# Performance work log

Measured on AMD Instinct MI355X. Metric: run time of the kernel, lower is better.

The kernel has to match this reference:

```python
import jax, jax.numpy as jnp
import numpy as np

N = 50000
E = 600000
HIDDEN = 128
HEADS = 4
HEAD_DIM = HIDDEN // HEADS
NEG_SLOPE = 0.2
LN_EPS = 1e-5


def setup_inputs() -> dict:
    key = jax.random.key(0)
    ks = jax.random.split(key, 16)
    s = 1.0 / np.sqrt(HIDDEN)
    inp = {
        "h": jax.random.normal(ks[0], (N, HIDDEN), dtype=jnp.float32),
        "src": jax.random.randint(ks[1], (E,), 0, N, dtype=jnp.int32),
        "dst": jax.random.randint(ks[2], (E,), 0, N, dtype=jnp.int32),
        # GATv2 params (share_weights=False, bias=True)
        "W_src": jax.random.normal(ks[3], (HIDDEN, HIDDEN), dtype=jnp.float32) * s,
        "b_src": jnp.zeros((HIDDEN,), dtype=jnp.float32),
        "W_dst": jax.random.normal(ks[4], (HIDDEN, HIDDEN), dtype=jnp.float32) * s,
        "b_dst": jnp.zeros((HIDDEN,), dtype=jnp.float32),
        "attn": jax.random.normal(ks[5], (HEADS, HEAD_DIM), dtype=jnp.float32) * s,
        # FFN params
        "W1": jax.random.normal(ks[6], (HIDDEN, 2 * HIDDEN), dtype=jnp.float32) * s,
        "bf1": jnp.zeros((2 * HIDDEN,), dtype=jnp.float32),
        "W2": jax.random.normal(ks[7], (2 * HIDDEN, HIDDEN), dtype=jnp.float32) * (1.0 / np.sqrt(2 * HIDDEN)),
        "bf2": jnp.zeros((HIDDEN,), dtype=jnp.float32),
        # LayerNorms
        "g1": jnp.ones((HIDDEN,), dtype=jnp.float32),
        "beta1": jnp.zeros((HIDDEN,), dtype=jnp.float32),
        "g2": jnp.ones((HIDDEN,), dtype=jnp.float32),
        "beta2": jnp.zeros((HIDDEN,), dtype=jnp.float32),
    }
    return inp


def _layernorm(x, g, b):
    mu = jnp.mean(x, axis=-1, keepdims=True)
    var = jnp.mean(jnp.square(x - mu), axis=-1, keepdims=True)
    return (x - mu) * jax.lax.rsqrt(var + LN_EPS) * g + b


def reference(h, src, dst, W_src, b_src, W_dst, b_dst, attn,
              W1, bf1, W2, bf2, g1, beta1, g2, beta2):
    # --- GATv2 attention (eval mode, dropouts are identity) ---
    fs = (h @ W_src + b_src).reshape(N, HEADS, HEAD_DIM)   # [N,H,D]
    fd = (h @ W_dst + b_dst).reshape(N, HEADS, HEAD_DIM)
    e = jax.nn.leaky_relu(fs[src] + fd[dst], NEG_SLOPE)    # [E,H,D]
    logits = jnp.einsum('ehd,hd->eh', e, attn)             # [E,H]
    # edge softmax over incoming edges of each dst node
    m = jax.ops.segment_max(logits, dst, num_segments=N)   # [N,H]
    m = jnp.where(jnp.isfinite(m), m, 0.0)                 # guard zero-in-degree
    a = jnp.exp(logits - m[dst])                           # [E,H]
    denom = jax.ops.segment_sum(a, dst, num_segments=N)    # [N,H]
    denom = jnp.where(denom == 0.0, 1.0, denom)
    alpha = a / denom[dst]                                 # [E,H]
    msg = fs[src] * alpha[:, :, None]                      # [E,H,D]
    rst = jax.ops.segment_sum(msg, dst, num_segments=N)    # [N,H,D]
    h_attn = rst.reshape(N, HIDDEN)
    # --- residual + LN, FFN + residual + LN ---
    h1 = _layernorm(h + h_attn, g1, beta1)
    ffn = jax.nn.gelu(h1 @ W1 + bf1, approximate=False) @ W2 + bf2
    out = _layernorm(h1 + ffn, g2, beta2)
    return out
```

## Files before the change

kernel.cpp:

```cpp
#include <hip/hip_runtime.h>
#include <math.h>

#define N_NODES 50000
#define N_EDGES 600000
#define HID 128
#define FFN_HID 256
#define NEG_SLOPE 0.2f
#define LN_EPS 1e-5f
#define BKT 64

typedef unsigned short u16;
typedef unsigned int u32;
typedef __attribute__((ext_vector_type(8))) short short8;
typedef __attribute__((ext_vector_type(4))) float floatx4;

__device__ __forceinline__ u16 f2bf(float x) {
    unsigned int u = __float_as_uint(x);
    unsigned int r = u + 0x7FFFu + ((u >> 16) & 1u);
    return (u16)(r >> 16);
}
__device__ __forceinline__ float bflo(u32 u) { return __uint_as_float(u << 16); }
__device__ __forceinline__ float bfhi(u32 u) { return __uint_as_float(u & 0xffff0000u); }
__device__ __forceinline__ u32 packbf(float lo, float hi) {
    return (u32)f2bf(lo) | ((u32)f2bf(hi) << 16);
}
__device__ __forceinline__ float gelu_fast(float v) {
    float u = 1.5957691216057308f * fmaf(0.044715f * v * v, v, v);
    return v / (1.0f + __expf(-u));
}


__global__ void scatter_prep(const int* __restrict__ src, const int* __restrict__ dst,
                             int* __restrict__ cursor, u16* __restrict__ ebkt,
                             const float* __restrict__ Wsrc, const float* __restrict__ Wdst,
                             const float* __restrict__ W1, const float* __restrict__ W2,
                             u16* __restrict__ B1, u16* __restrict__ B2, u16* __restrict__ B3) {
    int b = blockIdx.x;
    if (b < 2344) {
        int e = b * 256 + threadIdx.x;
        if (e < N_EDGES) {
            int d = dst[e];
            int slot = atomicAdd(&cursor[d], 1);
            if (slot < BKT) ebkt[(size_t)d * BKT + slot] = (u16)src[e];
        }
        return;
    }
    int t = (b - 2344) * 256 + threadIdx.x;
    const float* W; u16* out; int K, Nc, noff;
    if (t < 16384)       { W = Wsrc; out = B1; K = 128; Nc = 128; noff = 0; }
    else if (t < 32768)  { W = Wdst; out = B1; K = 128; Nc = 128; noff = 128; t -= 16384; }
    else if (t < 65536)  { W = W1;   out = B2; K = 128; Nc = 256; noff = 0;   t -= 32768; }
    else if (t < 98304)  { W = W2;   out = B3; K = 256; Nc = 128; noff = 0;   t -= 65536; }
    else return;
    int n = t % Nc, k = t / Nc;
    int ng = noff + n;
    int ksteps = K >> 5;
    int frag = (ng >> 4) * ksteps + (k >> 5);
    int lane = ((k >> 3) & 3) * 16 + (ng & 15);
    int j = k & 7;
    out[((size_t)frag * 64 + lane) * 8 + j] = f2bf(W[(size_t)k * Nc + n]);
}


__global__ __launch_bounds__(256) void gemm_fsfd_mfma(
    const float* __restrict__ h, const u16* __restrict__ Bsw,
    const float* __restrict__ bsrc, const float* __restrict__ bdst,
    u16* __restrict__ fsb, float* __restrict__ fdf)
{
    int tid = threadIdx.x, wave = tid >> 6, lane = tid & 63;
    int lrow = lane & 15, lq = lane >> 4;
    short8 bfrag[4][4];
    #pragma unroll
    for (int nt = 0; nt < 4; nt++)
        #pragma unroll
        for (int ks = 0; ks < 4; ks++) {
            int frag = (wave * 4 + nt) * 4 + ks;
            bfrag[nt][ks] = *(const short8*)(Bsw + ((size_t)frag * 64 + lane) * 8);
        }
    float bias[4];
    #pragma unroll
    for (int nt = 0; nt < 4; nt++) {
        int cg = wave * 64 + nt * 16 + lrow;
        bias[nt] = (cg < HID) ? bsrc[cg] : bdst[cg - HID];
    }
    for (int mb = blockIdx.x; mb < N_NODES / 16; mb += gridDim.x) {
        int m0 = mb * 16;
        const float* hrow = h + (size_t)(m0 + lrow) * HID;
        floatx4 acc[4];
        #pragma unroll
        for (int nt = 0; nt < 4; nt++) acc[nt] = {0.f, 0.f, 0.f, 0.f};
        #pragma unroll
        for (int ks = 0; ks < 4; ks++) {
            float4 va = *(const float4*)(hrow + ks * 32 + lq * 8);
            float4 vb = *(const float4*)(hrow + ks * 32 + lq * 8 + 4);
            short8 a;
            a[0] = (short)f2bf(va.x); a[1] = (short)f2bf(va.y);
            a[2] = (short)f2bf(va.z); a[3] = (short)f2bf(va.w);
            a[4] = (short)f2bf(vb.x); a[5] = (short)f2bf(vb.y);
            a[6] = (short)f2bf(vb.z); a[7] = (short)f2bf(vb.w);
            #pragma unroll
            for (int nt = 0; nt < 4; nt++)
                acc[nt] = __builtin_amdgcn_mfma_f32_16x16x32_bf16(a, bfrag[nt][ks], acc[nt], 0, 0, 0);
        }
        #pragma unroll
        for (int nt = 0; nt < 4; nt++) {
            int cg = wave * 64 + nt * 16 + lrow;
            if (cg < HID) {
                #pragma unroll
                for (int r = 0; r < 4; r++) {
                    int row = m0 + lq * 4 + r;
                    fsb[(size_t)row * HID + cg] = f2bf(acc[nt][r] + bias[nt]);
                }
            } else {
                #pragma unroll
                for (int r = 0; r < 4; r++) {
                    int row = m0 + lq * 4 + r;
                    fdf[(size_t)row * HID + cg - HID] = acc[nt][r] + bias[nt];
                }
            }
        }
    }
}


__global__ __launch_bounds__(256) void aggregate_kernel(
    const u16* __restrict__ fsb, const float* __restrict__ fdf,
    const float* __restrict__ h, const float* __restrict__ attn,
    const int* __restrict__ counts, const u16* __restrict__ ebkt,
    const float* __restrict__ g1, const float* __restrict__ beta1,
    float* __restrict__ h1f, u16* __restrict__ h1b)
{
    int wave = threadIdx.x >> 6, lane = threadIdx.x & 63;
    int node = blockIdx.x * 4 + wave;
    if (node >= N_NODES) return;
    int grp = lane >> 4, fl = lane & 15;
    int f = fl * 8;

    float4 d0 = *(const float4*)&fdf[(size_t)node * HID + f];
    float4 d1 = *(const float4*)&fdf[(size_t)node * HID + f + 4];
    float fdv[8] = { d0.x, d0.y, d0.z, d0.w, d1.x, d1.y, d1.z, d1.w };
    float4 aA = *(const float4*)&attn[f];
    float4 aB = *(const float4*)&attn[f + 4];
    float c1[8] = { 0.6f * aA.x, 0.6f * aA.y, 0.6f * aA.z, 0.6f * aA.w,
                    0.6f * aB.x, 0.6f * aB.y, 0.6f * aB.z, 0.6f * aB.w };
    float c2[8] = { 0.4f * aA.x, 0.4f * aA.y, 0.4f * aA.z, 0.4f * aA.w,
                    0.4f * aB.x, 0.4f * aB.y, 0.4f * aB.z, 0.4f * aB.w };

    int cnt = counts[node]; cnt = cnt < BKT ? cnt : BKT;
    const u16* brow = ebkt + (size_t)node * BKT;
    float acc[8] = {0.f, 0.f, 0.f, 0.f, 0.f, 0.f, 0.f, 0.f};
    float lsum = 0.f;

    auto body = [&](int e) {
        int s = (int)brow[e];
        uint4 u = *(const uint4*)&fsb[(size_t)s * HID + f];
        float x[8] = { bflo(u.x), bfhi(u.x), bflo(u.y), bfhi(u.y),
                       bflo(u.z), bfhi(u.z), bflo(u.w), bfhi(u.w) };
        float p = 0.f;
        #pragma unroll
        for (int i = 0; i < 8; i++) {
            float ei = x[i] + fdv[i];
            p = fmaf(c1[i], ei, p);
            p = fmaf(c2[i], fabsf(ei), p);
        }
        p += __shfl_xor(p, 1); p += __shfl_xor(p, 2);
        float w = __expf(p);
        lsum += w;
        #pragma unroll
        for (int i = 0; i < 8; i++) acc[i] = fmaf(w, x[i], acc[i]);
    };

    int e = grp;
    for (; e + 4 < cnt; e += 8) { body(e); body(e + 4); }
    if (e < cnt) body(e);

    #pragma unroll
    for (int i = 0; i < 8; i++) {
        acc[i] += __shfl_xor(acc[i], 16);
        acc[i] += __shfl_xor(acc[i], 32);
    }
    lsum += __shfl_xor(lsum, 16); lsum += __shfl_xor(lsum, 32);

    float inv = (lsum > 0.f) ? (1.0f / lsum) : 0.f;
    float4 h0 = *(const float4*)&h[(size_t)node * HID + f];
    float4 h1v = *(const float4*)&h[(size_t)node * HID + f + 4];
    float hx[8] = { h0.x, h0.y, h0.z, h0.w, h1v.x, h1v.y, h1v.z, h1v.w };
    float o[8], s1 = 0.f, s2 = 0.f;
    #pragma unroll
    for (int i = 0; i < 8; i++) {
        o[i] = hx[i] + acc[i] * inv;
        s1 += o[i]; s2 += o[i] * o[i];
    }
    s1 += __shfl_xor(s1, 1); s2 += __shfl_xor(s2, 1);
    s1 += __shfl_xor(s1, 2); s2 += __shfl_xor(s2, 2);
    s1 += __shfl_xor(s1, 4); s2 += __shfl_xor(s2, 4);
    s1 += __shfl_xor(s1, 8); s2 += __shfl_xor(s2, 8);
    float mu = s1 * (1.0f / HID);
    float var = s2 * (1.0f / HID) - mu * mu;
    float rs = rsqrtf(var + LN_EPS);
    if (grp == 0) {
        float4 gA = *(const float4*)&g1[f], gB = *(const float4*)&g1[f + 4];
        float4 bA = *(const float4*)&beta1[f], bB = *(const float4*)&beta1[f + 4];
        float q0 = (o[0] - mu) * rs * gA.x + bA.x, q1 = (o[1] - mu) * rs * gA.y + bA.y;
        float q2 = (o[2] - mu) * rs * gA.z + bA.z, q3 = (o[3] - mu) * rs * gA.w + bA.w;
        float q4 = (o[4] - mu) * rs * gB.x + bB.x, q5 = (o[5] - mu) * rs * gB.y + bB.y;
        float q6 = (o[6] - mu) * rs * gB.z + bB.z, q7 = (o[7] - mu) * rs * gB.w + bB.w;
        *(float4*)&h1f[(size_t)node * HID + f]     = make_float4(q0, q1, q2, q3);
        *(float4*)&h1f[(size_t)node * HID + f + 4] = make_float4(q4, q5, q6, q7);
        uint4 ob;
        ob.x = packbf(q0, q1); ob.y = packbf(q2, q3);
        ob.z = packbf(q4, q5); ob.w = packbf(q6, q7);
        *(uint4*)&h1b[(size_t)node * HID + f] = ob;
    }
}


#define TS_PAD 8

__global__ __launch_bounds__(256) void ffn_fused(
    const u16* __restrict__ h1b, const float* __restrict__ h1f,
    const u16* __restrict__ B2sw, const u16* __restrict__ B3sw,
    const float* __restrict__ bf1, const float* __restrict__ bf2,
    const float* __restrict__ g2, const float* __restrict__ beta2,
    float* __restrict__ out)
{
    __shared__ u16 ts[16][FFN_HID + TS_PAD];
    __shared__ float xs[16][HID];
    int tid = threadIdx.x, wave = tid >> 6, lane = tid & 63;
    int lrow = lane & 15, lq = lane >> 4;

    short8 b1f[4][4];
    #pragma unroll
    for (int nt = 0; nt < 4; nt++)
        #pragma unroll
        for (int ks = 0; ks < 4; ks++) {
            int frag = (wave * 4 + nt) * 4 + ks;
            b1f[nt][ks] = *(const short8*)(B2sw + ((size_t)frag * 64 + lane) * 8);
        }
    short8 b2f[2][8];
    #pragma unroll
    for (int nt = 0; nt < 2; nt++)
        #pragma unroll
        for (int ks = 0; ks < 8; ks++) {
            int frag = (wave * 2 + nt) * 8 + ks;
            b2f[nt][ks] = *(const short8*)(B3sw + ((size_t)frag * 64 + lane) * 8);
        }
    float bias1[4];
    #pragma unroll
    for (int nt = 0; nt < 4; nt++) bias1[nt] = bf1[wave * 64 + nt * 16 + lrow];
    float bias2[2];
    #pragma unroll
    for (int nt = 0; nt < 2; nt++) bias2[nt] = bf2[wave * 32 + nt * 16 + lrow];

    for (int mb = blockIdx.x; mb < N_NODES / 16; mb += gridDim.x) {
        int m0 = mb * 16;
        floatx4 acc1[4];
        #pragma unroll
        for (int nt = 0; nt < 4; nt++) acc1[nt] = {0.f, 0.f, 0.f, 0.f};
        #pragma unroll
        for (int ks = 0; ks < 4; ks++) {
            short8 a = *(const short8*)(h1b + (size_t)(m0 + lrow) * HID + ks * 32 + lq * 8);
            #pragma unroll
            for (int nt = 0; nt < 4; nt++)
                acc1[nt] = __builtin_amdgcn_mfma_f32_16x16x32_bf16(a, b1f[nt][ks], acc1[nt], 0, 0, 0);
        }
        #pragma unroll
        for (int nt = 0; nt < 4; nt++) {
            int cg = wave * 64 + nt * 16 + lrow;
            #pragma unroll
            for (int r = 0; r < 4; r++) {
                float v = acc1[nt][r] + bias1[nt];
                ts[lq * 4 + r][cg] = f2bf(gelu_fast(v));
            }
        }
        __syncthreads();
        floatx4 acc2[2];
        #pragma unroll
        for (int nt = 0; nt < 2; nt++) acc2[nt] = {0.f, 0.f, 0.f, 0.f};
        #pragma unroll
        for (int ks = 0; ks < 8; ks++) {
            short8 a = *(const short8*)&ts[lrow][ks * 32 + lq * 8];
            #pragma unroll
            for (int nt = 0; nt < 2; nt++)
                acc2[nt] = __builtin_amdgcn_mfma_f32_16x16x32_bf16(a, b2f[nt][ks], acc2[nt], 0, 0, 0);
        }
        #pragma unroll
        for (int nt = 0; nt < 2; nt++) {
            int cg = wave * 32 + nt * 16 + lrow;
            #pragma unroll
            for (int r = 0; r < 4; r++) {
                int row = m0 + lq * 4 + r;
                float resid = h1f[(size_t)row * HID + cg];
                xs[lq * 4 + r][cg] = acc2[nt][r] + bias2[nt] + resid;
            }
        }
        __syncthreads();
        int row = tid >> 4, c0 = (tid & 15) * 8;
        float v[8];
        float s1 = 0.f, s2 = 0.f;
        #pragma unroll
        for (int i = 0; i < 8; i++) { v[i] = xs[row][c0 + i]; s1 += v[i]; s2 += v[i] * v[i]; }
        s1 += __shfl_xor(s1, 1); s2 += __shfl_xor(s2, 1);
        s1 += __shfl_xor(s1, 2); s2 += __shfl_xor(s2, 2);
        s1 += __shfl_xor(s1, 4); s2 += __shfl_xor(s2, 4);
        s1 += __shfl_xor(s1, 8); s2 += __shfl_xor(s2, 8);
        float mu = s1 * (1.0f / HID);
        float var = s2 * (1.0f / HID) - mu * mu;
        float rs = rsqrtf(var + LN_EPS);
        float o[8];
        #pragma unroll
        for (int i = 0; i < 8; i++) o[i] = (v[i] - mu) * rs * g2[c0 + i] + beta2[c0 + i];
        float* op = out + (size_t)(m0 + row) * HID + c0;
        *(float4*)(op)     = make_float4(o[0], o[1], o[2], o[3]);
        *(float4*)(op + 4) = make_float4(o[4], o[5], o[6], o[7]);
        __syncthreads();
    }
}


extern "C" void kernel_launch(void* const* d_in, const int* in_sizes, int n_in,
                              void* d_out, int out_size, void* d_ws, size_t ws_size,
                              hipStream_t stream)
{
    const float* h    = (const float*)d_in[0];
    const int*   src  = (const int*)d_in[1];
    const int*   dst  = (const int*)d_in[2];
    const float* Wsrc = (const float*)d_in[3];
    const float* bsrc = (const float*)d_in[4];
    const float* Wdst = (const float*)d_in[5];
    const float* bdst = (const float*)d_in[6];
    const float* attn = (const float*)d_in[7];
    const float* W1   = (const float*)d_in[8];
    const float* bf1  = (const float*)d_in[9];
    const float* W2   = (const float*)d_in[10];
    const float* bf2  = (const float*)d_in[11];
    const float* g1   = (const float*)d_in[12];
    const float* beta1= (const float*)d_in[13];
    const float* g2   = (const float*)d_in[14];
    const float* beta2= (const float*)d_in[15];
    float* out = (float*)d_out;

    u16* fsb = (u16*)d_ws;
    float* fdf = (float*)(fsb + (size_t)N_NODES * HID);
    float* h1f = fdf + (size_t)N_NODES * HID;
    u16* h1b = (u16*)(h1f + (size_t)N_NODES * HID);
    u16* B1 = h1b + (size_t)N_NODES * HID;
    u16* B2 = B1 + 32768;
    u16* B3 = B2 + 32768;
    int* cursor = (int*)(B3 + 32768);
    u16* ebkt   = (u16*)(cursor + N_NODES);

    hipMemsetAsync(cursor, 0, N_NODES * sizeof(int), stream);
    scatter_prep<<<2728, 256, 0, stream>>>(src, dst, cursor, ebkt,
                                           Wsrc, Wdst, W1, W2, B1, B2, B3);
    gemm_fsfd_mfma<<<1024, 256, 0, stream>>>(h, B1, bsrc, bdst, fsb, fdf);
    aggregate_kernel<<<(N_NODES + 3) / 4, 256, 0, stream>>>(fsb, fdf, h, attn, cursor, ebkt, g1, beta1, h1f, h1b);
    ffn_fused<<<1563, 256, 0, stream>>>(h1b, h1f, B2, B3, bf1, bf2, g2, beta2, out);
}
```

Measured before the change: 237.4 us.

## Enlarge FFN row tile to 64 and apply LayerNorm in registers

The fused FFN kernel now handles 64 rows per tile instead of 16. Each block runs four 16-row sub-tiles through both MFMA GEMMs, so the per-block register load of weight fragments is amortized over more rows, and the grid shrinks to 391 blocks. The second LayerNorm now uses per-wave shuffle partial sums combined through a small shared array, replacing the staging of the full output tile in shared memory. The costs are a larger shared tile, more live registers, an unguarded partial last tile that reads past the end of h1b/h1f into other workspace, and narrower scalar output stores instead of float4.

```diff
diff --git a/kernel.cpp b/kernel.cpp
--- a/kernel.cpp
+++ b/kernel.cpp
@@ -216,6 +216,8 @@
 
 
 #define TS_PAD 8
+#define MTILE 64
+#define NTILES ((N_NODES + MTILE - 1) / MTILE)
 
 __global__ __launch_bounds__(256) void ffn_fused(
     const u16* __restrict__ h1b, const float* __restrict__ h1f,
@@ -224,8 +226,8 @@
     const float* __restrict__ g2, const float* __restrict__ beta2,
     float* __restrict__ out)
 {
-    __shared__ u16 ts[16][FFN_HID + TS_PAD];
-    __shared__ float xs[16][HID];
+    __shared__ u16 ts[MTILE][FFN_HID + TS_PAD];
+    __shared__ float part[MTILE][8];
     int tid = threadIdx.x, wave = tid >> 6, lane = tid & 63;
     int lrow = lane & 15, lq = lane >> 4;
 
@@ -248,71 +250,98 @@
     float bias1[4];
     #pragma unroll
     for (int nt = 0; nt < 4; nt++) bias1[nt] = bf1[wave * 64 + nt * 16 + lrow];
-    float bias2[2];
-    #pragma unroll
-    for (int nt = 0; nt < 2; nt++) bias2[nt] = bf2[wave * 32 + nt * 16 + lrow];
-
-    for (int mb = blockIdx.x; mb < N_NODES / 16; mb += gridDim.x) {
-        int m0 = mb * 16;
-        floatx4 acc1[4];
-        #pragma unroll
-        for (int nt = 0; nt < 4; nt++) acc1[nt] = {0.f, 0.f, 0.f, 0.f};
-        #pragma unroll
-        for (int ks = 0; ks < 4; ks++) {
-            short8 a = *(const short8*)(h1b + (size_t)(m0 + lrow) * HID + ks * 32 + lq * 8);
-            #pragma unroll
-            for (int nt = 0; nt < 4; nt++)
-                acc1[nt] = __builtin_amdgcn_mfma_f32_16x16x32_bf16(a, b1f[nt][ks], acc1[nt], 0, 0, 0);
-        }
-        #pragma unroll
-        for (int nt = 0; nt < 4; nt++) {
-            int cg = wave * 64 + nt * 16 + lrow;
+    float bias2[2], g2v[2], be2v[2];
+    #pragma unroll
+    for (int nt = 0; nt < 2; nt++) {
+        int cg = wave * 32 + nt * 16 + lrow;
+        bias2[nt] = bf2[cg]; g2v[nt] = g2[cg]; be2v[nt] = beta2[cg];
+    }
+
+    for (int mb = blockIdx.x; mb < NTILES; mb += gridDim.x) {
+        int m0 = mb * MTILE;
+        #pragma unroll
+        for (int rs = 0; rs < 4; rs++) {
+            floatx4 acc1[4];
+            #pragma unroll
+            for (int nt = 0; nt < 4; nt++) acc1[nt] = {0.f, 0.f, 0.f, 0.f};
+            #pragma unroll
+            for (int ks = 0; ks < 4; ks++) {
+                short8 a = *(const short8*)(h1b + (size_t)(m0 + rs * 16 + lrow) * HID + ks * 32 + lq * 8);
+                #pragma unroll
+                for (int nt = 0; nt < 4; nt++)
+                    acc1[nt] = __builtin_amdgcn_mfma_f32_16x16x32_bf16(a, b1f[nt][ks], acc1[nt], 0, 0, 0);
+            }
+            #pragma unroll
+            for (int nt = 0; nt < 4; nt++) {
+                int cg = wave * 64 + nt * 16 + lrow;
+                #pragma unroll
+                for (int r = 0; r < 4; r++) {
+                    float v = acc1[nt][r] + bias1[nt];
+                    ts[rs * 16 + lq * 4 + r][cg] = f2bf(gelu_fast(v));
+                }
+            }
+        }
+        __syncthreads();
+        float xv[4][2][4];
+        #pragma unroll
+        for (int rs = 0; rs < 4; rs++) {
+            floatx4 acc2[2];
+            #pragma unroll
+            for (int nt = 0; nt < 2; nt++) acc2[nt] = {0.f, 0.f, 0.f, 0.f};
+            #pragma unroll
+            for (int ks = 0; ks < 8; ks++) {
+                short8 a = *(const short8*)&ts[rs * 16 + lrow][ks * 32 + lq * 8];
+                #pragma unroll
+                for (int nt = 0; nt < 2; nt++)
+                    acc2[nt] = __builtin_amdgcn_mfma_f32_16x16x32_bf16(a, b2f[nt][ks], acc2[nt], 0, 0, 0);
+            }
+            #pragma unroll
+            for (int nt = 0; nt < 2; nt++) {
+                int cg = wave * 32 + nt * 16 + lrow;
+                #pragma unroll
+                for (int r = 0; r < 4; r++) {
+                    int row = m0 + rs * 16 + lq * 4 + r;
+                    xv[rs][nt][r] = acc2[nt][r] + bias2[nt] + h1f[(size_t)row * HID + cg];
+                }
+            }
             #pragma unroll
             for (int r = 0; r < 4; r++) {
-                float v = acc1[nt][r] + bias1[nt];
-                ts[lq * 4 + r][cg] = f2bf(gelu_fast(v));
+                float a0 = xv[rs][0][r], a1 = xv[rs][1][r];
+                float s1 = a0 + a1;
+                float s2 = a0 * a0 + a1 * a1;
+                s1 += __shfl_xor(s1, 1); s2 += __shfl_xor(s2, 1);
+                s1 += __shfl_xor(s1, 2); s2 += __shfl_xor(s2, 2);
+                s1 += __shfl_xor(s1, 4); s2 += __shfl_xor(s2, 4);
+                s1 += __shfl_xor(s1, 8); s2 += __shfl_xor(s2, 8);
+                if (lrow == 0) {
+                    part[rs * 16 + lq * 4 + r][wave * 2]     = s1;
+                    part[rs * 16 + lq * 4 + r][wave * 2 + 1] = s2;
+                }
             }
         }
         __syncthreads();
-        floatx4 acc2[2];
-        #pragma unroll
-        for (int nt = 0; nt < 2; nt++) acc2[nt] = {0.f, 0.f, 0.f, 0.f};
-        #pragma unroll
-        for (int ks = 0; ks < 8; ks++) {
-            short8 a = *(const short8*)&ts[lrow][ks * 32 + lq * 8];
-            #pragma unroll
-            for (int nt = 0; nt < 2; nt++)
-                acc2[nt] = __builtin_amdgcn_mfma_f32_16x16x32_bf16(a, b2f[nt][ks], acc2[nt], 0, 0, 0);
-        }
-        #pragma unroll
-        for (int nt = 0; nt < 2; nt++) {
-            int cg = wave * 32 + nt * 16 + lrow;
+        #pragma unroll
+        for (int rs = 0; rs < 4; rs++) {
             #pragma unroll
             for (int r = 0; r < 4; r++) {
-                int row = m0 + lq * 4 + r;
-                float resid = h1f[(size_t)row * HID + cg];
-                xs[lq * 4 + r][cg] = acc2[nt][r] + bias2[nt] + resid;
-            }
-        }
-        __syncthreads();
-        int row = tid >> 4, c0 = (tid & 15) * 8;
-        float v[8];
-        float s1 = 0.f, s2 = 0.f;
-        #pragma unroll
-        for (int i = 0; i < 8; i++) { v[i] = xs[row][c0 + i]; s1 += v[i]; s2 += v[i] * v[i]; }
-        s1 += __shfl_xor(s1, 1); s2 += __shfl_xor(s2, 1);
-        s1 += __shfl_xor(s1, 2); s2 += __shfl_xor(s2, 2);
-        s1 += __shfl_xor(s1, 4); s2 += __shfl_xor(s2, 4);
-        s1 += __shfl_xor(s1, 8); s2 += __shfl_xor(s2, 8);
-        float mu = s1 * (1.0f / HID);
-        float var = s2 * (1.0f / HID) - mu * mu;
-        float rs = rsqrtf(var + LN_EPS);
-        float o[8];
-        #pragma unroll
-        for (int i = 0; i < 8; i++) o[i] = (v[i] - mu) * rs * g2[c0 + i] + beta2[c0 + i];
-        float* op = out + (size_t)(m0 + row) * HID + c0;
-        *(float4*)(op)     = make_float4(o[0], o[1], o[2], o[3]);
-        *(float4*)(op + 4) = make_float4(o[4], o[5], o[6], o[7]);
+                int rloc = rs * 16 + lq * 4 + r;
+                int row = m0 + rloc;
+                float4 p0 = *(const float4*)&part[rloc][0];
+                float4 p1 = *(const float4*)&part[rloc][4];
+                float s1 = (p0.x + p0.z) + (p1.x + p1.z);
+                float s2 = (p0.y + p0.w) + (p1.y + p1.w);
+                float mu = s1 * (1.0f / HID);
+                float var = s2 * (1.0f / HID) - mu * mu;
+                float rstd = rsqrtf(var + LN_EPS);
+                if (row < N_NODES) {
+                    #pragma unroll
+                    for (int nt = 0; nt < 2; nt++) {
+                        int cg = wave * 32 + nt * 16 + lrow;
+                        out[(size_t)row * HID + cg] = (xv[rs][nt][r] - mu) * rstd * g2v[nt] + be2v[nt];
+                    }
+                }
+            }
+        }
         __syncthreads();
     }
 }
@@ -355,5 +384,5 @@
                                            Wsrc, Wdst, W1, W2, B1, B2, B3);
     gemm_fsfd_mfma<<<1024, 256, 0, stream>>>(h, B1, bsrc, bdst, fsb, fdf);
     aggregate_kernel<<<(N_NODES + 3) / 4, 256, 0, stream>>>(fsb, fdf, h, attn, cursor, ebkt, g1, beta1, h1f, h1b);
-    ffn_fused<<<1563, 256, 0, stream>>>(h1b, h1f, B2, B3, bf1, bf2, g2, beta2, out);
-}
+    ffn_fused<<<391, 256, 0, stream>>>(h1b, h1f, B2, B3, bf1, bf2, g2, beta2, out);
+}
```

Result: slower. 243.1 us (+2.4%).

## Split fused FFN into two wave-per-tile kernels with LDS-staged weights

Applied to the files above, without the earlier changes.

Replaces the single fused FFN kernel, where four waves cooperated on a 16-row tile through LDS with syncs, with two kernels. Each wave now owns a full 16-row tile and computes all output columns, reading the swizzled weight fragments from a 64KB LDS copy. The GELU intermediate goes to a bf16 global buffer that reuses the fdf workspace, and LayerNorm is done in registers with shuffles. This removes the intra-block barriers and the LDS round trips for the intermediate and residual. In exchange it adds a global write and read of the intermediate, reloads 64KB of weights per block, and the large LDS footprint may limit occupancy.

```diff
diff --git a/kernel.cpp b/kernel.cpp
--- a/kernel.cpp
+++ b/kernel.cpp
@@ -215,105 +215,101 @@
 }
 
 
-#define TS_PAD 8
-
-__global__ __launch_bounds__(256) void ffn_fused(
-    const u16* __restrict__ h1b, const float* __restrict__ h1f,
-    const u16* __restrict__ B2sw, const u16* __restrict__ B3sw,
-    const float* __restrict__ bf1, const float* __restrict__ bf2,
+#define FF_TILES (N_NODES / 16)
+
+__global__ __launch_bounds__(256) void ffn1_kernel(
+    const u16* __restrict__ h1b, const u16* __restrict__ B2sw,
+    const float* __restrict__ bf1, u16* __restrict__ tbuf)
+{
+    __shared__ u16 bs[32768];
+    for (int i = threadIdx.x; i < 4096; i += 256)
+        *(uint4*)(bs + (size_t)i * 8) = *(const uint4*)(B2sw + (size_t)i * 8);
+    __syncthreads();
+    int wave = threadIdx.x >> 6, lane = threadIdx.x & 63;
+    int lrow = lane & 15, lq = lane >> 4;
+    int tile = blockIdx.x * 4 + wave;
+    if (tile >= FF_TILES) return;
+    int m0 = tile * 16;
+
+    floatx4 acc[16];
+    #pragma unroll
+    for (int nt = 0; nt < 16; nt++) acc[nt] = {0.f, 0.f, 0.f, 0.f};
+    #pragma unroll
+    for (int ks = 0; ks < 4; ks++) {
+        short8 a = *(const short8*)(h1b + (size_t)(m0 + lrow) * HID + ks * 32 + lq * 8);
+        #pragma unroll
+        for (int nt = 0; nt < 16; nt++) {
+            short8 b = *(const short8*)&bs[((nt * 4 + ks) * 64 + lane) * 8];
+            acc[nt] = __builtin_amdgcn_mfma_f32_16x16x32_bf16(a, b, acc[nt], 0, 0, 0);
+        }
+    }
+    #pragma unroll
+    for (int nt = 0; nt < 16; nt++) {
+        float bias = bf1[nt * 16 + lrow];
+        #pragma unroll
+        for (int r = 0; r < 4; r++) {
+            float v = acc[nt][r] + bias;
+            tbuf[(size_t)(m0 + lq * 4 + r) * FFN_HID + nt * 16 + lrow] = f2bf(gelu_fast(v));
+        }
+    }
+}
+
+__global__ __launch_bounds__(256) void ffn2_kernel(
+    const u16* __restrict__ tbuf, const float* __restrict__ h1f,
+    const u16* __restrict__ B3sw, const float* __restrict__ bf2,
     const float* __restrict__ g2, const float* __restrict__ beta2,
     float* __restrict__ out)
 {
-    __shared__ u16 ts[16][FFN_HID + TS_PAD];
-    __shared__ float xs[16][HID];
-    int tid = threadIdx.x, wave = tid >> 6, lane = tid & 63;
+    __shared__ u16 bs[32768];
+    for (int i = threadIdx.x; i < 4096; i += 256)
+        *(uint4*)(bs + (size_t)i * 8) = *(const uint4*)(B3sw + (size_t)i * 8);
+    __syncthreads();
+    int wave = threadIdx.x >> 6, lane = threadIdx.x & 63;
     int lrow = lane & 15, lq = lane >> 4;
-
-    short8 b1f[4][4];
-    #pragma unroll
-    for (int nt = 0; nt < 4; nt++)
-        #pragma unroll
-        for (int ks = 0; ks < 4; ks++) {
-            int frag = (wave * 4 + nt) * 4 + ks;
-            b1f[nt][ks] = *(const short8*)(B2sw + ((size_t)frag * 64 + lane) * 8);
-        }
-    short8 b2f[2][8];
-    #pragma unroll
-    for (int nt = 0; nt < 2; nt++)
-        #pragma unroll
-        for (int ks = 0; ks < 8; ks++) {
-            int frag = (wave * 2 + nt) * 8 + ks;
-            b2f[nt][ks] = *(const short8*)(B3sw + ((size_t)frag * 64 + lane) * 8);
-        }
-    float bias1[4];
-    #pragma unroll
-    for (int nt = 0; nt < 4; nt++) bias1[nt] = bf1[wave * 64 + nt * 16 + lrow];
-    float bias2[2];
-    #pragma unroll
-    for (int nt = 0; nt < 2; nt++) bias2[nt] = bf2[wave * 32 + nt * 16 + lrow];
-
-    for (int mb = blockIdx.x; mb < N_NODES / 16; mb += gridDim.x) {
-        int m0 = mb * 16;
-        floatx4 acc1[4];
-        #pragma unroll
-        for (int nt = 0; nt < 4; nt++) acc1[nt] = {0.f, 0.f, 0.f, 0.f};
-        #pragma unroll
-        for (int ks = 0; ks < 4; ks++) {
-            short8 a = *(const short8*)(h1b + (size_t)(m0 + lrow) * HID + ks * 32 + lq * 8);
-            #pragma unroll
-            for (int nt = 0; nt < 4; nt++)
-                acc1[nt] = __builtin_amdgcn_mfma_f32_16x16x32_bf16(a, b1f[nt][ks], acc1[nt], 0, 0, 0);
-        }
-        #pragma unroll
-        for (int nt = 0; nt < 4; nt++) {
-            int cg = wave * 64 + nt * 16 + lrow;
-            #pragma unroll
-            for (int r = 0; r < 4; r++) {
-                float v = acc1[nt][r] + bias1[nt];
-                ts[lq * 4 + r][cg] = f2bf(gelu_fast(v));
-            }
-        }
-        __syncthreads();
-        floatx4 acc2[2];
-        #pragma unroll
-        for (int nt = 0; nt < 2; nt++) acc2[nt] = {0.f, 0.f, 0.f, 0.f};
-        #pragma unroll
-        for (int ks = 0; ks < 8; ks++) {
-            short8 a = *(const short8*)&ts[lrow][ks * 32 + lq * 8];
-            #pragma unroll
-            for (int nt = 0; nt < 2; nt++)
-                acc2[nt] = __builtin_amdgcn_mfma_f32_16x16x32_bf16(a, b2f[nt][ks], acc2[nt], 0, 0, 0);
-        }
-        #pragma unroll
-        for (int nt = 0; nt < 2; nt++) {
-            int cg = wave * 32 + nt * 16 + lrow;
-            #pragma unroll
-            for (int r = 0; r < 4; r++) {
-                int row = m0 + lq * 4 + r;
-                float resid = h1f[(size_t)row * HID + cg];
-                xs[lq * 4 + r][cg] = acc2[nt][r] + bias2[nt] + resid;
-            }
-        }
-        __syncthreads();
-        int row = tid >> 4, c0 = (tid & 15) * 8;
-        float v[8];
+    int tile = blockIdx.x * 4 + wave;
+    if (tile >= FF_TILES) return;
+    int m0 = tile * 16;
+
+    floatx4 acc[8];
+    #pragma unroll
+    for (int nt = 0; nt < 8; nt++) acc[nt] = {0.f, 0.f, 0.f, 0.f};
+    #pragma unroll
+    for (int ks = 0; ks < 8; ks++) {
+        short8 a = *(const short8*)(tbuf + (size_t)(m0 + lrow) * FFN_HID + ks * 32 + lq * 8);
+        #pragma unroll
+        for (int nt = 0; nt < 8; nt++) {
+            short8 b = *(const short8*)&bs[((nt * 8 + ks) * 64 + lane) * 8];
+            acc[nt] = __builtin_amdgcn_mfma_f32_16x16x32_bf16(a, b, acc[nt], 0, 0, 0);
+        }
+    }
+    float xv[8][4];
+    #pragma unroll
+    for (int nt = 0; nt < 8; nt++) {
+        float bias = bf2[nt * 16 + lrow];
+        #pragma unroll
+        for (int r = 0; r < 4; r++) {
+            int row = m0 + lq * 4 + r;
+            xv[nt][r] = acc[nt][r] + bias + h1f[(size_t)row * HID + nt * 16 + lrow];
+        }
+    }
+    #pragma unroll
+    for (int r = 0; r < 4; r++) {
         float s1 = 0.f, s2 = 0.f;
         #pragma unroll
-        for (int i = 0; i < 8; i++) { v[i] = xs[row][c0 + i]; s1 += v[i]; s2 += v[i] * v[i]; }
+        for (int nt = 0; nt < 8; nt++) { s1 += xv[nt][r]; s2 += xv[nt][r] * xv[nt][r]; }
         s1 += __shfl_xor(s1, 1); s2 += __shfl_xor(s2, 1);
         s1 += __shfl_xor(s1, 2); s2 += __shfl_xor(s2, 2);
         s1 += __shfl_xor(s1, 4); s2 += __shfl_xor(s2, 4);
         s1 += __shfl_xor(s1, 8); s2 += __shfl_xor(s2, 8);
         float mu = s1 * (1.0f / HID);
         float var = s2 * (1.0f / HID) - mu * mu;
-        float rs = rsqrtf(var + LN_EPS);
-        float o[8];
-        #pragma unroll
-        for (int i = 0; i < 8; i++) o[i] = (v[i] - mu) * rs * g2[c0 + i] + beta2[c0 + i];
-        float* op = out + (size_t)(m0 + row) * HID + c0;
-        *(float4*)(op)     = make_float4(o[0], o[1], o[2], o[3]);
-        *(float4*)(op + 4) = make_float4(o[4], o[5], o[6], o[7]);
-        __syncthreads();
+        float rstd = rsqrtf(var + LN_EPS);
+        int row = m0 + lq * 4 + r;
+        #pragma unroll
+        for (int nt = 0; nt < 8; nt++) {
+            int cg = nt * 16 + lrow;
+            out[(size_t)row * HID + cg] = (xv[nt][r] - mu) * rstd * g2[cg] + beta2[cg];
+        }
     }
 }
 
@@ -349,11 +345,13 @@
     u16* B3 = B2 + 32768;
     int* cursor = (int*)(B3 + 32768);
     u16* ebkt   = (u16*)(cursor + N_NODES);
+    u16* tbuf   = (u16*)fdf;
 
     hipMemsetAsync(cursor, 0, N_NODES * sizeof(int), stream);
     scatter_prep<<<2728, 256, 0, stream>>>(src, dst, cursor, ebkt,
                                            Wsrc, Wdst, W1, W2, B1, B2, B3);
     gemm_fsfd_mfma<<<1024, 256, 0, stream>>>(h, B1, bsrc, bdst, fsb, fdf);
     aggregate_kernel<<<(N_NODES + 3) / 4, 256, 0, stream>>>(fsb, fdf, h, attn, cursor, ebkt, g1, beta1, h1f, h1b);
-    ffn_fused<<<1563, 256, 0, stream>>>(h1b, h1f, B2, B3, bf1, bf2, g2, beta2, out);
-}
+    ffn1_kernel<<<(FF_TILES + 3) / 4, 256, 0, stream>>>(h1b, B2, bf1, tbuf);
+    ffn2_kernel<<<(FF_TILES + 3) / 4, 256, 0, stream>>>(tbuf, h1f, B3, bf2, g2, beta2, out);
+}
```

After: 252.4 us. 6.3% more time.

## Fuse edge scatter into projection GEMM and store intermediates in bf16

Applied to the files above, without the earlier changes.

Edge bucketing now runs inside the same launch as the source/destination projection GEMM, and weight swizzling moves to its own small kernel. The fd projection is stored as bf16, the fp32 h1 copy is dropped so the FFN residual reads from the bf16 h1, and atomic counters are padded to a 16-int stride to reduce contention on shared cache lines. This cuts intermediate memory traffic and launch overlap gaps, at the cost of lower precision in the attention logits and the residual, and a larger memset. The FFN grid shrinks to 640 blocks.

```diff
diff --git a/kernel.cpp b/kernel.cpp
--- a/kernel.cpp
+++ b/kernel.cpp
@@ -8,6 +8,7 @@
 #define NEG_SLOPE 0.2f
 #define LN_EPS 1e-5f
 #define BKT 64
+#define CSTR 16
 
 typedef unsigned short u16;
 typedef unsigned int u32;
@@ -24,28 +25,19 @@
 __device__ __forceinline__ u32 packbf(float lo, float hi) {
     return (u32)f2bf(lo) | ((u32)f2bf(hi) << 16);
 }
+__device__ __forceinline__ float bf2f(u16 v) { return __uint_as_float(((u32)v) << 16); }
 __device__ __forceinline__ float gelu_fast(float v) {
     float u = 1.5957691216057308f * fmaf(0.044715f * v * v, v, v);
     return v / (1.0f + __expf(-u));
 }
 
 
-__global__ void scatter_prep(const int* __restrict__ src, const int* __restrict__ dst,
-                             int* __restrict__ cursor, u16* __restrict__ ebkt,
-                             const float* __restrict__ Wsrc, const float* __restrict__ Wdst,
-                             const float* __restrict__ W1, const float* __restrict__ W2,
-                             u16* __restrict__ B1, u16* __restrict__ B2, u16* __restrict__ B3) {
-    int b = blockIdx.x;
-    if (b < 2344) {
-        int e = b * 256 + threadIdx.x;
-        if (e < N_EDGES) {
-            int d = dst[e];
-            int slot = atomicAdd(&cursor[d], 1);
-            if (slot < BKT) ebkt[(size_t)d * BKT + slot] = (u16)src[e];
-        }
-        return;
-    }
-    int t = (b - 2344) * 256 + threadIdx.x;
+__global__ __launch_bounds__(256) void swizzle_prep(
+    const float* __restrict__ Wsrc, const float* __restrict__ Wdst,
+    const float* __restrict__ W1, const float* __restrict__ W2,
+    u16* __restrict__ B1, u16* __restrict__ B2, u16* __restrict__ B3)
+{
+    int t = blockIdx.x * 256 + threadIdx.x;
     const float* W; u16* out; int K, Nc, noff;
     if (t < 16384)       { W = Wsrc; out = B1; K = 128; Nc = 128; noff = 0; }
     else if (t < 32768)  { W = Wdst; out = B1; K = 128; Nc = 128; noff = 128; t -= 16384; }
@@ -62,11 +54,23 @@
 }
 
 
-__global__ __launch_bounds__(256) void gemm_fsfd_mfma(
+__global__ __launch_bounds__(256) void scatter_gemm(
+    const int* __restrict__ src, const int* __restrict__ dst,
+    int* __restrict__ cursor, u16* __restrict__ ebkt,
     const float* __restrict__ h, const u16* __restrict__ Bsw,
     const float* __restrict__ bsrc, const float* __restrict__ bdst,
-    u16* __restrict__ fsb, float* __restrict__ fdf)
-{
+    u16* __restrict__ fsb, u16* __restrict__ fdb)
+{
+    if (blockIdx.x < 2344) {
+        int e = blockIdx.x * 256 + threadIdx.x;
+        if (e < N_EDGES) {
+            int d = dst[e];
+            int slot = atomicAdd(&cursor[d * CSTR], 1);
+            if (slot < BKT) ebkt[(size_t)d * BKT + slot] = (u16)src[e];
+        }
+        return;
+    }
+    int bid = blockIdx.x - 2344;
     int tid = threadIdx.x, wave = tid >> 6, lane = tid & 63;
     int lrow = lane & 15, lq = lane >> 4;
     short8 bfrag[4][4];
@@ -83,7 +87,7 @@
         int cg = wave * 64 + nt * 16 + lrow;
         bias[nt] = (cg < HID) ? bsrc[cg] : bdst[cg - HID];
     }
-    for (int mb = blockIdx.x; mb < N_NODES / 16; mb += gridDim.x) {
+    for (int mb = bid; mb < N_NODES / 16; mb += 1024) {
         int m0 = mb * 16;
         const float* hrow = h + (size_t)(m0 + lrow) * HID;
         floatx4 acc[4];
@@ -105,18 +109,12 @@
         #pragma unroll
         for (int nt = 0; nt < 4; nt++) {
             int cg = wave * 64 + nt * 16 + lrow;
-            if (cg < HID) {
-                #pragma unroll
-                for (int r = 0; r < 4; r++) {
-                    int row = m0 + lq * 4 + r;
-                    fsb[(size_t)row * HID + cg] = f2bf(acc[nt][r] + bias[nt]);
-                }
-            } else {
-                #pragma unroll
-                for (int r = 0; r < 4; r++) {
-                    int row = m0 + lq * 4 + r;
-                    fdf[(size_t)row * HID + cg - HID] = acc[nt][r] + bias[nt];
-                }
+            u16* outp = (cg < HID) ? fsb : fdb;
+            int c = cg & (HID - 1);
+            #pragma unroll
+            for (int r = 0; r < 4; r++) {
+                int row = m0 + lq * 4 + r;
+                outp[(size_t)row * HID + c] = f2bf(acc[nt][r] + bias[nt]);
             }
         }
     }
@@ -124,11 +122,11 @@
 
 
 __global__ __launch_bounds__(256) void aggregate_kernel(
-    const u16* __restrict__ fsb, const float* __restrict__ fdf,
+    const u16* __restrict__ fsb, const u16* __restrict__ fdb,
     const float* __restrict__ h, const float* __restrict__ attn,
-    const int* __restrict__ counts, const u16* __restrict__ ebkt,
+    const int* __restrict__ cursor, const u16* __restrict__ ebkt,
     const float* __restrict__ g1, const float* __restrict__ beta1,
-    float* __restrict__ h1f, u16* __restrict__ h1b)
+    u16* __restrict__ h1b)
 {
     int wave = threadIdx.x >> 6, lane = threadIdx.x & 63;
     int node = blockIdx.x * 4 + wave;
@@ -136,9 +134,9 @@
     int grp = lane >> 4, fl = lane & 15;
     int f = fl * 8;
 
-    float4 d0 = *(const float4*)&fdf[(size_t)node * HID + f];
-    float4 d1 = *(const float4*)&fdf[(size_t)node * HID + f + 4];
-    float fdv[8] = { d0.x, d0.y, d0.z, d0.w, d1.x, d1.y, d1.z, d1.w };
+    uint4 ud = *(const uint4*)&fdb[(size_t)node * HID + f];
+    float fdv[8] = { bflo(ud.x), bfhi(ud.x), bflo(ud.y), bfhi(ud.y),
+                     bflo(ud.z), bfhi(ud.z), bflo(ud.w), bfhi(ud.w) };
     float4 aA = *(const float4*)&attn[f];
     float4 aB = *(const float4*)&attn[f + 4];
     float c1[8] = { 0.6f * aA.x, 0.6f * aA.y, 0.6f * aA.z, 0.6f * aA.w,
@@ -146,7 +144,7 @@
     float c2[8] = { 0.4f * aA.x, 0.4f * aA.y, 0.4f * aA.z, 0.4f * aA.w,
                     0.4f * aB.x, 0.4f * aB.y, 0.4f * aB.z, 0.4f * aB.w };
 
-    int cnt = counts[node]; cnt = cnt < BKT ? cnt : BKT;
+    int cnt = cursor[node * CSTR]; cnt = cnt < BKT ? cnt : BKT;
     const u16* brow = ebkt + (size_t)node * BKT;
     float acc[8] = {0.f, 0.f, 0.f, 0.f, 0.f, 0.f, 0.f, 0.f};
     float lsum = 0.f;
@@ -205,8 +203,6 @@
         float q2 = (o[2] - mu) * rs * gA.z + bA.z, q3 = (o[3] - mu) * rs * gA.w + bA.w;
         float q4 = (o[4] - mu) * rs * gB.x + bB.x, q5 = (o[5] - mu) * rs * gB.y + bB.y;
         float q6 = (o[6] - mu) * rs * gB.z + bB.z, q7 = (o[7] - mu) * rs * gB.w + bB.w;
-        *(float4*)&h1f[(size_t)node * HID + f]     = make_float4(q0, q1, q2, q3);
-        *(float4*)&h1f[(size_t)node * HID + f + 4] = make_float4(q4, q5, q6, q7);
         uint4 ob;
         ob.x = packbf(q0, q1); ob.y = packbf(q2, q3);
         ob.z = packbf(q4, q5); ob.w = packbf(q6, q7);
@@ -218,7 +214,7 @@
 #define TS_PAD 8
 
 __global__ __launch_bounds__(256) void ffn_fused(
-    const u16* __restrict__ h1b, const float* __restrict__ h1f,
+    const u16* __restrict__ h1b,
     const u16* __restrict__ B2sw, const u16* __restrict__ B3sw,
     const float* __restrict__ bf1, const float* __restrict__ bf2,
     const float* __restrict__ g2, const float* __restrict__ beta2,
@@ -290,7 +286,7 @@
             #pragma unroll
             for (int r = 0; r < 4; r++) {
                 int row = m0 + lq * 4 + r;
-                float resid = h1f[(size_t)row * HID + cg];
+                float resid = bf2f(h1b[(size_t)row * HID + cg]);
                 xs[lq * 4 + r][cg] = acc2[nt][r] + bias2[nt] + resid;
             }
         }
@@ -341,19 +337,18 @@
     float* out = (float*)d_out;
 
     u16* fsb = (u16*)d_ws;
-    float* fdf = (float*)(fsb + (size_t)N_NODES * HID);
-    float* h1f = fdf + (size_t)N_NODES * HID;
-    u16* h1b = (u16*)(h1f + (size_t)N_NODES * HID);
+    u16* fdb = fsb + (size_t)N_NODES * HID;
+    u16* h1b = fdb + (size_t)N_NODES * HID;
     u16* B1 = h1b + (size_t)N_NODES * HID;
     u16* B2 = B1 + 32768;
     u16* B3 = B2 + 32768;
     int* cursor = (int*)(B3 + 32768);
-    u16* ebkt   = (u16*)(cursor + N_NODES);
-
-    hipMemsetAsync(cursor, 0, N_NODES * sizeof(int), stream);
-    scatter_prep<<<2728, 256, 0, stream>>>(src, dst, cursor, ebkt,
-                                           Wsrc, Wdst, W1, W2, B1, B2, B3);
-    gemm_fsfd_mfma<<<1024, 256, 0, stream>>>(h, B1, bsrc, bdst, fsb, fdf);
-    aggregate_kernel<<<(N_NODES + 3) / 4, 256, 0, stream>>>(fsb, fdf, h, attn, cursor, ebkt, g1, beta1, h1f, h1b);
-    ffn_fused<<<1563, 256, 0, stream>>>(h1b, h1f, B2, B3, bf1, bf2, g2, beta2, out);
-}
+    u16* ebkt   = (u16*)(cursor + (size_t)N_NODES * CSTR);
+
+    hipMemsetAsync(cursor, 0, (size_t)N_NODES * CSTR * sizeof(int), stream);
+    swizzle_prep<<<384, 256, 0, stream>>>(Wsrc, Wdst, W1, W2, B1, B2, B3);
+    scatter_gemm<<<2344 + 1024, 256, 0, stream>>>(src, dst, cursor, ebkt,
+                                                  h, B1, bsrc, bdst, fsb, fdb);
+    aggregate_kernel<<<(N_NODES + 3) / 4, 256, 0, stream>>>(fsb, fdb, h, attn, cursor, ebkt, g1, beta1, h1b);
+    ffn_fused<<<640, 256, 0, stream>>>(h1b, B2, B3, bf1, bf2, g2, beta2, out);
+}
```

Measured after the change: 232.4 us. 1.02x faster.
